# Optimization experiments

Hardware: AMD Instinct MI355X
Metric: run time of the kernel (lower is better)

## Reference

```python
import jax, jax.numpy as jnp
import numpy as np

N = 50000   # nodes
E = 800000  # edges
G = 64      # graphs in batch
H = 64      # hidden_dim
IN = 4      # input_dim (degree-derived features)


def setup_inputs() -> dict:
    key = jax.random.key(0)
    ks = jax.random.split(key, 9)
    src = jax.random.randint(ks[0], (E,), 0, N, dtype=jnp.int32)
    dst = jax.random.randint(ks[1], (E,), 0, N, dtype=jnp.int32)
    graph_ids = jnp.sort(jax.random.randint(ks[2], (N,), 0, G, dtype=jnp.int32))

    def glorot(k, shape):
        fan_in = shape[0]
        return jax.random.normal(k, shape, jnp.float32) / np.float32(np.sqrt(fan_in))

    return dict(
        src=src, dst=dst, graph_ids=graph_ids,
        W1=glorot(ks[3], (IN, H)), b1=jnp.zeros((H,), jnp.float32),
        W2=glorot(ks[4], (H, H)),  b2=jnp.zeros((H,), jnp.float32),
        W3=glorot(ks[5], (H, H)),  b3=jnp.zeros((H,), jnp.float32),
        W4=glorot(ks[6], (H, H)),  b4=jnp.zeros((H,), jnp.float32),
        Wout=glorot(ks[7], (H, 1)), bout=jnp.zeros((1,), jnp.float32),
    )


def _graph_conv(h, src, dst, norm_src, norm_dst, W, b):
    # DGL GraphConv, norm='both': D_dst^{-1/2} * A^T * (D_src^{-1/2} * h) @ W + b
    m = (h * norm_src)[src]                              # [E, F] gather
    agg = jax.ops.segment_sum(m, dst, num_segments=N)    # [N, F] scatter-add
    return (agg * norm_dst) @ W + b


def reference(src, dst, graph_ids, W1, b1, W2, b2, W3, b3, W4, b4, Wout, bout):
    ones_e = jnp.ones((E,), jnp.float32)
    in_deg = jax.ops.segment_sum(ones_e, dst, num_segments=N)   # [N]
    out_deg = jax.ops.segment_sum(ones_e, src, num_segments=N)  # [N]

    # degree-derived node features (exactly as in forward)
    h1 = in_deg[:, None]
    h2 = (in_deg - 3.0 > 0).astype(jnp.float32)[:, None]
    h3 = 3.0 / h1
    h4 = (in_deg - 4.0 > 0).astype(jnp.float32)[:, None]
    h_ = jnp.concatenate([h1, h2, h3, h4], axis=1)               # [N, 4]

    # symmetric norms (DGL clamps degree to >= 1)
    norm_src = jnp.clip(out_deg, 1.0, None)[:, None] ** -0.5     # [N, 1]
    norm_dst = jnp.clip(in_deg, 1.0, None)[:, None] ** -0.5      # [N, 1]

    h = jax.nn.relu(_graph_conv(h_, src, dst, norm_src, norm_dst, W1, b1))
    h = jax.nn.relu(_graph_conv(h, src, dst, norm_src, norm_dst, W2, b2))
    h = jax.nn.relu(_graph_conv(h, src, dst, norm_src, norm_dst, W3, b3))
    h = jax.nn.relu(_graph_conv(h, src, dst, norm_src, norm_dst, W4, b4))

    # dgl.mean_nodes: per-graph mean pooling
    node_counts = jax.ops.segment_sum(jnp.ones((N,), jnp.float32), graph_ids, num_segments=G)
    graph_emb = jax.ops.segment_sum(h, graph_ids, num_segments=G) / node_counts[:, None]

    # dropout = identity at inference
    return jax.nn.sigmoid(graph_emb @ Wout + bout)               # [G, 1]
```

## Files before the change

### kernel.cpp

```cpp
#include <hip/hip_runtime.h>
#include <hip/hip_fp8.h>
#include <math.h>

#define N_NODES 50000
#define N_EDGES 800000
#define NP 8
#define NS 64
#define PSZ (N_NODES / NP)
#define SSZ (N_EDGES / NS)
#define NB 196

typedef _Float16 half8 __attribute__((ext_vector_type(8)));
typedef float floatx4 __attribute__((ext_vector_type(4)));

__device__ __forceinline__ unsigned char f_to_fp8(float f) {
    __hip_fp8_e4m3 q(f);
    return (unsigned char)q.__x;
}
__device__ __forceinline__ float fp8_to_f(unsigned char u) {
    __hip_fp8_e4m3 q;
    q.__x = (__hip_fp8_storage_t)u;
    return (float)q;
}

__global__ __launch_bounds__(256) void hist_wt_kernel(const int* __restrict__ src,
                                                      const int* __restrict__ dst,
                                                      unsigned char* __restrict__ inpart,
                                                      unsigned char* __restrict__ outpart,
                                                      unsigned char* __restrict__ rank,
                                                      const float* __restrict__ W2,
                                                      const float* __restrict__ W3,
                                                      const float* __restrict__ W4,
                                                      _Float16* __restrict__ WT,
                                                      float* __restrict__ gacc) {
    __shared__ int h[PSZ + 2];
    if (blockIdx.x >= NP * NS) {
        int wb = blockIdx.x - NP * NS;
        if (wb < 48) {
            int i = wb * 256 + threadIdx.x;
            if (i < 3 * 4096) {
                int l = i >> 12;
                int r = i & 4095;
                int k = r >> 6, n = r & 63;
                const float* W = (l == 0) ? W2 : (l == 1) ? W3 : W4;
                WT[l * 4096 + n * 64 + k] = (_Float16)W[r];
            }
        } else {
            for (int i = threadIdx.x; i < 64 * 64 + 64; i += 256) gacc[i] = 0.0f;
        }
        return;
    }
    int p = blockIdx.x / NS, s = blockIdx.x % NS;
    for (int i = threadIdx.x; i < (PSZ + 2) / 4 + 1; i += 256)
        if (4 * i < PSZ + 2) ((int4*)h)[i] = make_int4(0, 0, 0, 0);
    __syncthreads();
    int lo = p * PSZ;
    int ebase = s * SSZ;
    const int4* d4 = (const int4*)(dst + ebase);
    const int4* s4 = (const int4*)(src + ebase);
    unsigned char* rk = rank + ebase;
    for (int i = threadIdx.x; i < SSZ / 4; i += 256) {
        int4 d = d4[i];
        int4 sv = s4[i];
        int t;
        t = d.x - lo;  if ((unsigned)t < PSZ) rk[4 * i + 0] = (unsigned char)(atomicAdd(&h[t], 1) & 0xffff);
        t = d.y - lo;  if ((unsigned)t < PSZ) rk[4 * i + 1] = (unsigned char)(atomicAdd(&h[t], 1) & 0xffff);
        t = d.z - lo;  if ((unsigned)t < PSZ) rk[4 * i + 2] = (unsigned char)(atomicAdd(&h[t], 1) & 0xffff);
        t = d.w - lo;  if ((unsigned)t < PSZ) rk[4 * i + 3] = (unsigned char)(atomicAdd(&h[t], 1) & 0xffff);
        t = sv.x - lo; if ((unsigned)t < PSZ) atomicAdd(&h[t], 0x10000);
        t = sv.y - lo; if ((unsigned)t < PSZ) atomicAdd(&h[t], 0x10000);
        t = sv.z - lo; if ((unsigned)t < PSZ) atomicAdd(&h[t], 0x10000);
        t = sv.w - lo; if ((unsigned)t < PSZ) atomicAdd(&h[t], 0x10000);
    }
    __syncthreads();
    unsigned char* ip = inpart + (size_t)s * N_NODES + lo;
    unsigned char* op = outpart + (size_t)s * N_NODES + lo;
    for (int i = threadIdx.x; i < PSZ / 2; i += 256) {
        int v0 = h[2 * i], v1 = h[2 * i + 1];
        uchar2 iv, ov;
        iv.x = (unsigned char)(v0 & 0xff);
        iv.y = (unsigned char)(v1 & 0xff);
        ov.x = (unsigned char)((v0 >> 16) & 0xff);
        ov.y = (unsigned char)((v1 >> 16) & 0xff);
        ((uchar2*)ip)[i] = iv;
        ((uchar2*)op)[i] = ov;
    }
}

__global__ void scan_block_feat_kernel(unsigned char* __restrict__ inpart,
                                       const unsigned char* __restrict__ outpart,
                                       const int* __restrict__ graph_ids,
                                       int* __restrict__ row_start, int* __restrict__ blk_sums,
                                       float* __restrict__ norm_src, float* __restrict__ norm_dst,
                                       uchar4* __restrict__ hs0, float* __restrict__ gcnt, int N) {
    __shared__ int ghist[64];
    if (threadIdx.x < 64) ghist[threadIdx.x] = 0;
    int i = blockIdx.x * 256 + threadIdx.x;
    int din_i = 0, dout_i = 0;
    if (i < N) {
        unsigned char run = 0;
#pragma unroll
        for (int s = 0; s < NS; ++s) {
            unsigned char c = inpart[(size_t)s * N_NODES + i];
            inpart[(size_t)s * N_NODES + i] = run;
            run = (unsigned char)(run + c);
            dout_i += outpart[(size_t)s * N_NODES + i];
        }
        din_i = (int)run;
        float din = (float)din_i;
        float dout = (float)dout_i;
        float ns = 1.0f / sqrtf(fmaxf(dout, 1.0f));
        float nd = 1.0f / sqrtf(fmaxf(din, 1.0f));
        norm_src[i] = ns;
        norm_dst[i] = nd;
        float h1 = din;
        float h2 = (din - 3.0f > 0.0f) ? 1.0f : 0.0f;
        float h3 = 3.0f / din;
        float h4 = (din - 4.0f > 0.0f) ? 1.0f : 0.0f;
        uchar4 q;
        q.x = f_to_fp8(h1 * ns);
        q.y = f_to_fp8(h2 * ns);
        q.z = f_to_fp8(h3 * ns);
        q.w = f_to_fp8(h4 * ns);
        hs0[i] = q;
    }
    __syncthreads();
    if (i < N) atomicAdd(&ghist[graph_ids[i]], 1);
    int lane = threadIdx.x & 63;
    int wid = threadIdx.x >> 6;
    int x = din_i;
#pragma unroll
    for (int off = 1; off < 64; off <<= 1) {
        int t = __shfl_up(x, off);
        if (lane >= off) x += t;
    }
    __shared__ int wsum[4];
    if (lane == 63) wsum[wid] = x;
    __syncthreads();
    int woff = 0;
    for (int w = 0; w < wid; ++w) woff += wsum[w];
    int incl = x + woff;
    if (i < N) row_start[i] = incl - din_i;
    if (threadIdx.x == 255) blk_sums[blockIdx.x] = incl;
    if (threadIdx.x < 64 && ghist[threadIdx.x] > 0)
        atomicAdd(&gcnt[threadIdx.x], (float)ghist[threadIdx.x]);
}

__global__ void row_add_kernel(int* __restrict__ row_start,
                               const int* __restrict__ blk_sums, int N) {
    __shared__ int sOff[256];
    int t = threadIdx.x;
    int v = (t < NB) ? blk_sums[t] : 0;
    int lane = t & 63;
    int wid = t >> 6;
    int x = v;
#pragma unroll
    for (int off = 1; off < 64; off <<= 1) {
        int tt = __shfl_up(x, off);
        if (lane >= off) x += tt;
    }
    __shared__ int wsum[4];
    if (lane == 63) wsum[wid] = x;
    __syncthreads();
    int woff = 0;
    for (int w = 0; w < wid; ++w) woff += wsum[w];
    sOff[t] = x + woff - v;
    __syncthreads();
    int i = blockIdx.x * 256 + threadIdx.x;
    if (blockIdx.x == 0 && threadIdx.x == 0) row_start[N] = N_EDGES;
    if (i < N) row_start[i] += sOff[blockIdx.x];
}

__global__ __launch_bounds__(256) void csr_fill_kernel(const int* __restrict__ src,
                                                       const int* __restrict__ dst,
                                                       const int* __restrict__ row_start,
                                                       const unsigned char* __restrict__ inpart,
                                                       const unsigned char* __restrict__ rank,
                                                       int* __restrict__ csr_src) {
    int i = blockIdx.x * 256 + threadIdx.x;
    if (i >= N_EDGES / 4) return;
    int4 d = ((const int4*)dst)[i];
    int4 sv = ((const int4*)src)[i];
    uchar4 rk = ((const uchar4*)rank)[i];
    int s = (4 * i) / SSZ;
    const unsigned char* pref = inpart + (size_t)s * N_NODES;
    csr_src[row_start[d.x] + (int)pref[d.x] + (int)rk.x] = sv.x;
    csr_src[row_start[d.y] + (int)pref[d.y] + (int)rk.y] = sv.y;
    csr_src[row_start[d.z] + (int)pref[d.z] + (int)rk.z] = sv.z;
    csr_src[row_start[d.w] + (int)pref[d.w] + (int)rk.w] = sv.w;
}

__global__ void conv4_kernel(const uchar4* __restrict__ hs0,
                             const int* __restrict__ row_start,
                             const int* __restrict__ csr_src,
                             const float* __restrict__ norm_src,
                             const float* __restrict__ norm_dst,
                             const float* __restrict__ W, const float* __restrict__ b,
                             unsigned char* __restrict__ out, int N) {
    __shared__ float sW[4 * 64];
    __shared__ float sb[64];
    sW[threadIdx.x] = W[threadIdx.x];
    if (threadIdx.x < 64) sb[threadIdx.x] = b[threadIdx.x];
    __syncthreads();
    int lane = threadIdx.x & 63;
    int wid = threadIdx.x >> 6;
    int v = blockIdx.x * 4 + wid;
    if (v >= N) return;
    int rs = row_start[v], re = row_start[v + 1];
    float ax = 0.f, ay = 0.f, az = 0.f, aw = 0.f;
    for (int e = rs + lane; e < re; e += 64) {
        uchar4 f = hs0[csr_src[e]];
        ax += fp8_to_f(f.x); ay += fp8_to_f(f.y);
        az += fp8_to_f(f.z); aw += fp8_to_f(f.w);
    }
#pragma unroll
    for (int off = 32; off; off >>= 1) {
        ax += __shfl_xor(ax, off);
        ay += __shfl_xor(ay, off);
        az += __shfl_xor(az, off);
        aw += __shfl_xor(aw, off);
    }
    float nd = norm_dst[v];
    float r = sb[lane] + nd * (ax * sW[lane] + ay * sW[64 + lane] +
                               az * sW[128 + lane] + aw * sW[192 + lane]);
    r = fmaxf(r, 0.0f) * norm_src[v];
    out[(size_t)v * 64 + lane] = f_to_fp8(r);
}

#define LOADIDX(MY, E0)  MY = csr_src[(E0) + (lane & 15)];

#define GATHER(T, MY)                                                   \
    _Pragma("unroll")                                                   \
    for (int j = 0; j < 16; ++j) {                                      \
        unsigned uu = (unsigned)__builtin_amdgcn_readlane(MY, j);       \
        if (uu >= (unsigned)N_NODES) uu = 0;                            \
        T[j] = hs_in[(uu << 6) + (unsigned)lane];                       \
    }

#define ACCUM(T)                                                        \
    _Pragma("unroll")                                                   \
    for (int j = 0; j < 16; ++j) {                                      \
        while (ecur == bound) {                                         \
            float ndc = __uint_as_float(                                \
                (unsigned)__builtin_amdgcn_readlane((int)nd8u, cur - vbase)); \
            sAgg[wavei][cur - vbase][lane] = (_Float16)(acc * ndc);     \
            acc = 0.0f;                                                 \
            ++cur;                                                      \
            bound = (cur < vend)                                        \
                        ? __builtin_amdgcn_readlane(rb8, cur - vbase)   \
                        : 0x7fffffff;                                   \
        }                                                               \
        acc += fp8_to_f(T[j]);                                          \
        ++ecur;                                                         \
    }

__global__ __launch_bounds__(256) void conv64_kernel(
        const unsigned char* __restrict__ hs_in,
        const int* __restrict__ row_start,
        const int* __restrict__ csr_src,
        const float* __restrict__ norm_src,
        const float* __restrict__ norm_dst,
        const _Float16* __restrict__ WT, const float* __restrict__ b,
        unsigned char* __restrict__ out8,
        const int* __restrict__ graph_ids, float* __restrict__ gacc,
        int do_pool, int N) {
    __shared__ _Float16 sAgg[4][16][72];
    const int lane = threadIdx.x & 63;
    const int wavei = __builtin_amdgcn_readfirstlane(threadIdx.x >> 6);
    const int vbase = blockIdx.x * 32 + wavei * 8;
    if (vbase >= N) return;

    const int vend = vbase + 8;
    const int rb8 = row_start[vbase + 1 + (lane & 7)];
    const unsigned nd8u = __float_as_uint(norm_dst[vbase + (lane & 7)]);
    const unsigned ns8u = __float_as_uint(norm_src[vbase + (lane & 7)]);
    const int rs = row_start[vbase];
    const int re = __builtin_amdgcn_readlane(rb8, 7);
    int cur = vbase;
    int bound = __builtin_amdgcn_readlane(rb8, 0);
    int ecur = rs;
    float acc = 0.0f;
    int nbp = (re - rs + 15) >> 4;
    int e = rs;
    int myA, myB;
    unsigned char tA[16], tB[16];

    if (nbp > 0) {
        LOADIDX(myA, e);
        GATHER(tA, myA);
        LOADIDX(myB, e + 16);
        int k = 0;
        while (k + 2 <= nbp) {
            GATHER(tB, myB);
            LOADIDX(myA, e + 32);
            ACCUM(tA);
            if (k + 2 < nbp) {
                GATHER(tA, myA);
                LOADIDX(myB, e + 48);
            }
            ACCUM(tB);
            k += 2; e += 32;
        }
        if (k < nbp) { ACCUM(tA); }
    }
    while (cur < vend) {
        float ndc = __uint_as_float(
            (unsigned)__builtin_amdgcn_readlane((int)nd8u, cur - vbase));
        sAgg[wavei][cur - vbase][lane] = (_Float16)(acc * ndc);
        acc = 0.0f;
        ++cur;
    }

    const int l15 = lane & 15;
    const int quad = lane >> 4;
    const _Float16* aRow = &sAgg[wavei][l15][quad * 8];
    half8 a0 = *(const half8*)(aRow);
    half8 a1 = *(const half8*)(aRow + 32);

    floatx4 c[4];
#pragma unroll
    for (int nt = 0; nt < 4; ++nt) c[nt] = (floatx4){0.f, 0.f, 0.f, 0.f};

#pragma unroll
    for (int nt = 0; nt < 4; ++nt) {
        const _Float16* bp = WT + ((size_t)(nt * 16 + l15)) * 64 + quad * 8;
        half8 b0 = *(const half8*)bp;
        half8 b1 = *(const half8*)(bp + 32);
        c[nt] = __builtin_amdgcn_mfma_f32_16x16x32_f16(a0, b0, c[nt], 0, 0, 0);
        c[nt] = __builtin_amdgcn_mfma_f32_16x16x32_f16(a1, b1, c[nt], 0, 0, 0);
    }

    if (do_pool) {
        int g0 = graph_ids[vbase];
        int g7 = graph_ids[vbase + 7];
        if (g0 == g7) {
#pragma unroll
            for (int nt = 0; nt < 4; ++nt) {
                float bias = b[nt * 16 + l15];
                float fsum = 0.0f;
                if (quad < 2) {
#pragma unroll
                    for (int r = 0; r < 4; ++r)
                        fsum += fmaxf(c[nt][r] + bias, 0.0f);
                }
                fsum += __shfl_xor(fsum, 16);
                if (quad == 0)
                    atomicAdd(&gacc[g0 * 64 + nt * 16 + l15], fsum);
            }
        } else {
#pragma unroll
            for (int nt = 0; nt < 4; ++nt) {
                float bias = b[nt * 16 + l15];
#pragma unroll
                for (int r = 0; r < 4; ++r) {
                    int m = quad * 4 + r;
                    if (m < 8) {
                        int v = vbase + m;
                        float val = fmaxf(c[nt][r] + bias, 0.0f);
                        atomicAdd(&gacc[graph_ids[v] * 64 + nt * 16 + l15], val);
                    }
                }
            }
        }
    } else {
#pragma unroll
        for (int nt = 0; nt < 4; ++nt) {
            float bias = b[nt * 16 + l15];
#pragma unroll
            for (int r = 0; r < 4; ++r) {
                int m = quad * 4 + r;
                int v = vbase + m;
                if (m < 8 && v < N) {
                    float nsv = __uint_as_float(
                        (unsigned)__builtin_amdgcn_readlane((int)ns8u, m));
                    float val = fmaxf(c[nt][r] + bias, 0.0f) * nsv;
                    out8[(size_t)v * 64 + nt * 16 + l15] = f_to_fp8(val);
                }
            }
        }
    }
}

__global__ void pool2_kernel(const float* __restrict__ gacc, const float* __restrict__ gcnt,
                             const float* __restrict__ Wout, const float* __restrict__ bout,
                             float* __restrict__ out) {
    int lane = threadIdx.x & 63;
    int g = blockIdx.x * 4 + (threadIdx.x >> 6);
    float p = (gacc[g * 64 + lane] / gcnt[g]) * Wout[lane];
#pragma unroll
    for (int off = 32; off; off >>= 1) p += __shfl_xor(p, off);
    if (lane == 0) out[g] = 1.0f / (1.0f + expf(-(p + bout[0])));
}

extern "C" void kernel_launch(void* const* d_in, const int* in_sizes, int n_in,
                              void* d_out, int out_size, void* d_ws, size_t ws_size,
                              hipStream_t stream) {
    const int* src = (const int*)d_in[0];
    const int* dst = (const int*)d_in[1];
    const int* graph_ids = (const int*)d_in[2];
    const float* W1 = (const float*)d_in[3];
    const float* b1 = (const float*)d_in[4];
    const float* W2 = (const float*)d_in[5];
    const float* b2 = (const float*)d_in[6];
    const float* W3 = (const float*)d_in[7];
    const float* b3 = (const float*)d_in[8];
    const float* W4 = (const float*)d_in[9];
    const float* b4 = (const float*)d_in[10];
    const float* Wout = (const float*)d_in[11];
    const float* bout = (const float*)d_in[12];
    float* out = (float*)d_out;

    const int N = N_NODES, E = N_EDGES;

    unsigned char* buf8A = (unsigned char*)d_ws;
    unsigned char* buf8B = buf8A + (size_t)N * 64;
    _Float16* WT   = (_Float16*)(buf8B + (size_t)N * 64);
    float* gacc = (float*)(WT + 3 * 4096);
    float* gcnt = gacc + 64 * 64;
    unsigned char* hs0 = (unsigned char*)(gcnt + 64);
    float* norm_src = (float*)(hs0 + (size_t)N * 4);
    float* norm_dst = norm_src + N;
    int* csr_src   = (int*)(norm_dst + N);
    int* row_start = csr_src + E;
    int* blk_sums  = row_start + (N + 1);
    unsigned char* inpart  = (unsigned char*)(blk_sums + NB + 1);
    unsigned char* outpart = inpart + (size_t)NS * N;
    unsigned char* rank    = outpart + (size_t)NS * N;

    hist_wt_kernel<<<NP * NS + 49, 256, 0, stream>>>(src, dst, inpart, outpart, rank,
                                                     W2, W3, W4, WT, gacc);
    scan_block_feat_kernel<<<NB, 256, 0, stream>>>(inpart, outpart, graph_ids,
                                                   row_start, blk_sums,
                                                   norm_src, norm_dst, (uchar4*)hs0, gcnt, N);
    row_add_kernel<<<NB, 256, 0, stream>>>(row_start, blk_sums, N);
    csr_fill_kernel<<<(E / 4 + 255) / 256, 256, 0, stream>>>(src, dst, row_start, inpart,
                                                             rank, csr_src);

    conv4_kernel<<<(N + 3) / 4, 256, 0, stream>>>((const uchar4*)hs0, row_start, csr_src,
                                                  norm_src, norm_dst, W1, b1, buf8A, N);
    const int CB = (N + 31) / 32;
    conv64_kernel<<<CB, 256, 0, stream>>>(buf8A, row_start, csr_src, norm_src, norm_dst,
                                          WT + 0 * 4096, b2, buf8B, graph_ids, gacc, 0, N);
    conv64_kernel<<<CB, 256, 0, stream>>>(buf8B, row_start, csr_src, norm_src, norm_dst,
                                          WT + 1 * 4096, b3, buf8A, graph_ids, gacc, 0, N);
    conv64_kernel<<<CB, 256, 0, stream>>>(buf8A, row_start, csr_src, norm_src, norm_dst,
                                          WT + 2 * 4096, b4, (unsigned char*)nullptr,
                                          graph_ids, gacc, 1, N);

    pool2_kernel<<<16, 256, 0, stream>>>(gacc, gcnt, Wout, bout, out);
}
```

Baseline: 212.5 us.

## Replace partitioned LDS histogram CSR build with global atomic counting and fill

Drops the partitioned shared-memory histogram with per-slice byte counts and ranks. Degrees are now counted with global atomics, and the CSR fill claims slots with atomicAdd on a write pointer array. A memset now zeroes the accumulators and degree arrays, and the scan reads degrees directly instead of walking 64 slices. This removes a large LDS-zeroing phase and the per-slice prefix work, but relies on contended global atomics and makes the neighbor order inside each row nondeterministic.

Measured after the change: 300.2 us. 1.41x slower.

```diff
diff --git a/kernel.cpp b/kernel.cpp
--- a/kernel.cpp
+++ b/kernel.cpp
@@ -4,11 +4,8 @@
 
 #define N_NODES 50000
 #define N_EDGES 800000
-#define NP 8
-#define NS 64
-#define PSZ (N_NODES / NP)
-#define SSZ (N_EDGES / NS)
 #define NB 196
+#define EQB 782
 
 typedef _Float16 half8 __attribute__((ext_vector_type(8)));
 typedef float floatx4 __attribute__((ext_vector_type(4)));
@@ -23,90 +20,52 @@
     return (float)q;
 }
 
-__global__ __launch_bounds__(256) void hist_wt_kernel(const int* __restrict__ src,
-                                                      const int* __restrict__ dst,
-                                                      unsigned char* __restrict__ inpart,
-                                                      unsigned char* __restrict__ outpart,
-                                                      unsigned char* __restrict__ rank,
-                                                      const float* __restrict__ W2,
-                                                      const float* __restrict__ W3,
-                                                      const float* __restrict__ W4,
-                                                      _Float16* __restrict__ WT,
-                                                      float* __restrict__ gacc) {
-    __shared__ int h[PSZ + 2];
-    if (blockIdx.x >= NP * NS) {
-        int wb = blockIdx.x - NP * NS;
-        if (wb < 48) {
-            int i = wb * 256 + threadIdx.x;
-            if (i < 3 * 4096) {
-                int l = i >> 12;
-                int r = i & 4095;
-                int k = r >> 6, n = r & 63;
-                const float* W = (l == 0) ? W2 : (l == 1) ? W3 : W4;
-                WT[l * 4096 + n * 64 + k] = (_Float16)W[r];
-            }
-        } else {
-            for (int i = threadIdx.x; i < 64 * 64 + 64; i += 256) gacc[i] = 0.0f;
+__global__ __launch_bounds__(256) void count_wt_kernel(const int* __restrict__ src,
+                                                       const int* __restrict__ dst,
+                                                       int* __restrict__ deg_in,
+                                                       int* __restrict__ deg_out,
+                                                       const float* __restrict__ W2,
+                                                       const float* __restrict__ W3,
+                                                       const float* __restrict__ W4,
+                                                       _Float16* __restrict__ WT) {
+    if (blockIdx.x >= EQB) {
+        int i = (blockIdx.x - EQB) * 256 + threadIdx.x;
+        if (i < 3 * 4096) {
+            int l = i >> 12;
+            int r = i & 4095;
+            int k = r >> 6, n = r & 63;
+            const float* W = (l == 0) ? W2 : (l == 1) ? W3 : W4;
+            WT[l * 4096 + n * 64 + k] = (_Float16)W[r];
         }
         return;
     }
-    int p = blockIdx.x / NS, s = blockIdx.x % NS;
-    for (int i = threadIdx.x; i < (PSZ + 2) / 4 + 1; i += 256)
-        if (4 * i < PSZ + 2) ((int4*)h)[i] = make_int4(0, 0, 0, 0);
-    __syncthreads();
-    int lo = p * PSZ;
-    int ebase = s * SSZ;
-    const int4* d4 = (const int4*)(dst + ebase);
-    const int4* s4 = (const int4*)(src + ebase);
-    unsigned char* rk = rank + ebase;
-    for (int i = threadIdx.x; i < SSZ / 4; i += 256) {
-        int4 d = d4[i];
-        int4 sv = s4[i];
-        int t;
-        t = d.x - lo;  if ((unsigned)t < PSZ) rk[4 * i + 0] = (unsigned char)(atomicAdd(&h[t], 1) & 0xffff);
-        t = d.y - lo;  if ((unsigned)t < PSZ) rk[4 * i + 1] = (unsigned char)(atomicAdd(&h[t], 1) & 0xffff);
-        t = d.z - lo;  if ((unsigned)t < PSZ) rk[4 * i + 2] = (unsigned char)(atomicAdd(&h[t], 1) & 0xffff);
-        t = d.w - lo;  if ((unsigned)t < PSZ) rk[4 * i + 3] = (unsigned char)(atomicAdd(&h[t], 1) & 0xffff);
-        t = sv.x - lo; if ((unsigned)t < PSZ) atomicAdd(&h[t], 0x10000);
-        t = sv.y - lo; if ((unsigned)t < PSZ) atomicAdd(&h[t], 0x10000);
-        t = sv.z - lo; if ((unsigned)t < PSZ) atomicAdd(&h[t], 0x10000);
-        t = sv.w - lo; if ((unsigned)t < PSZ) atomicAdd(&h[t], 0x10000);
-    }
-    __syncthreads();
-    unsigned char* ip = inpart + (size_t)s * N_NODES + lo;
-    unsigned char* op = outpart + (size_t)s * N_NODES + lo;
-    for (int i = threadIdx.x; i < PSZ / 2; i += 256) {
-        int v0 = h[2 * i], v1 = h[2 * i + 1];
-        uchar2 iv, ov;
-        iv.x = (unsigned char)(v0 & 0xff);
-        iv.y = (unsigned char)(v1 & 0xff);
-        ov.x = (unsigned char)((v0 >> 16) & 0xff);
-        ov.y = (unsigned char)((v1 >> 16) & 0xff);
-        ((uchar2*)ip)[i] = iv;
-        ((uchar2*)op)[i] = ov;
-    }
-}
-
-__global__ void scan_block_feat_kernel(unsigned char* __restrict__ inpart,
-                                       const unsigned char* __restrict__ outpart,
-                                       const int* __restrict__ graph_ids,
-                                       int* __restrict__ row_start, int* __restrict__ blk_sums,
-                                       float* __restrict__ norm_src, float* __restrict__ norm_dst,
-                                       uchar4* __restrict__ hs0, float* __restrict__ gcnt, int N) {
+    int i = blockIdx.x * 256 + threadIdx.x;
+    if (i >= N_EDGES / 4) return;
+    int4 d = ((const int4*)dst)[i];
+    int4 s = ((const int4*)src)[i];
+    atomicAdd(&deg_in[d.x], 1);
+    atomicAdd(&deg_in[d.y], 1);
+    atomicAdd(&deg_in[d.z], 1);
+    atomicAdd(&deg_in[d.w], 1);
+    atomicAdd(&deg_out[s.x], 1);
+    atomicAdd(&deg_out[s.y], 1);
+    atomicAdd(&deg_out[s.z], 1);
+    atomicAdd(&deg_out[s.w], 1);
+}
+
+__global__ void feat_scan_kernel(const int* __restrict__ deg_in,
+                                 const int* __restrict__ deg_out,
+                                 const int* __restrict__ graph_ids,
+                                 int* __restrict__ row_start, int* __restrict__ blk_sums,
+                                 float* __restrict__ norm_src, float* __restrict__ norm_dst,
+                                 uchar4* __restrict__ hs0, float* __restrict__ gcnt, int N) {
     __shared__ int ghist[64];
     if (threadIdx.x < 64) ghist[threadIdx.x] = 0;
     int i = blockIdx.x * 256 + threadIdx.x;
-    int din_i = 0, dout_i = 0;
+    int din_i = 0;
     if (i < N) {
-        unsigned char run = 0;
-#pragma unroll
-        for (int s = 0; s < NS; ++s) {
-            unsigned char c = inpart[(size_t)s * N_NODES + i];
-            inpart[(size_t)s * N_NODES + i] = run;
-            run = (unsigned char)(run + c);
-            dout_i += outpart[(size_t)s * N_NODES + i];
-        }
-        din_i = (int)run;
+        din_i = deg_in[i];
+        int dout_i = deg_out[i];
         float din = (float)din_i;
         float dout = (float)dout_i;
         float ns = 1.0f / sqrtf(fmaxf(dout, 1.0f));
@@ -147,7 +106,8 @@
 }
 
 __global__ void row_add_kernel(int* __restrict__ row_start,
-                               const int* __restrict__ blk_sums, int N) {
+                               const int* __restrict__ blk_sums,
+                               int* __restrict__ wptr, int N) {
     __shared__ int sOff[256];
     int t = threadIdx.x;
     int v = (t < NB) ? blk_sums[t] : 0;
@@ -168,26 +128,25 @@
     __syncthreads();
     int i = blockIdx.x * 256 + threadIdx.x;
     if (blockIdx.x == 0 && threadIdx.x == 0) row_start[N] = N_EDGES;
-    if (i < N) row_start[i] += sOff[blockIdx.x];
-}
-
-__global__ __launch_bounds__(256) void csr_fill_kernel(const int* __restrict__ src,
-                                                       const int* __restrict__ dst,
-                                                       const int* __restrict__ row_start,
-                                                       const unsigned char* __restrict__ inpart,
-                                                       const unsigned char* __restrict__ rank,
-                                                       int* __restrict__ csr_src) {
+    if (i < N) {
+        int rv = row_start[i] + sOff[blockIdx.x];
+        row_start[i] = rv;
+        wptr[i] = rv;
+    }
+}
+
+__global__ __launch_bounds__(256) void fill_kernel(const int* __restrict__ src,
+                                                   const int* __restrict__ dst,
+                                                   int* __restrict__ wptr,
+                                                   int* __restrict__ csr_src) {
     int i = blockIdx.x * 256 + threadIdx.x;
     if (i >= N_EDGES / 4) return;
     int4 d = ((const int4*)dst)[i];
     int4 sv = ((const int4*)src)[i];
-    uchar4 rk = ((const uchar4*)rank)[i];
-    int s = (4 * i) / SSZ;
-    const unsigned char* pref = inpart + (size_t)s * N_NODES;
-    csr_src[row_start[d.x] + (int)pref[d.x] + (int)rk.x] = sv.x;
-    csr_src[row_start[d.y] + (int)pref[d.y] + (int)rk.y] = sv.y;
-    csr_src[row_start[d.z] + (int)pref[d.z] + (int)rk.z] = sv.z;
-    csr_src[row_start[d.w] + (int)pref[d.w] + (int)rk.w] = sv.w;
+    csr_src[atomicAdd(&wptr[d.x], 1)] = sv.x;
+    csr_src[atomicAdd(&wptr[d.y], 1)] = sv.y;
+    csr_src[atomicAdd(&wptr[d.z], 1)] = sv.z;
+    csr_src[atomicAdd(&wptr[d.w], 1)] = sv.w;
 }
 
 __global__ void conv4_kernel(const uchar4* __restrict__ hs0,
@@ -415,26 +374,27 @@
     unsigned char* buf8A = (unsigned char*)d_ws;
     unsigned char* buf8B = buf8A + (size_t)N * 64;
     _Float16* WT   = (_Float16*)(buf8B + (size_t)N * 64);
-    float* gacc = (float*)(WT + 3 * 4096);
-    float* gcnt = gacc + 64 * 64;
-    unsigned char* hs0 = (unsigned char*)(gcnt + 64);
+    float* gacc    = (float*)(WT + 3 * 4096);
+    float* gcnt    = gacc + 64 * 64;
+    int*   deg_in  = (int*)(gcnt + 64);
+    int*   deg_out = deg_in + N;
+    size_t zbytes  = (size_t)(64 * 64 + 64 + 2 * N) * 4;
+    int*   wptr    = deg_out + N;
+    unsigned char* hs0 = (unsigned char*)(wptr + N);
     float* norm_src = (float*)(hs0 + (size_t)N * 4);
     float* norm_dst = norm_src + N;
     int* csr_src   = (int*)(norm_dst + N);
     int* row_start = csr_src + E;
     int* blk_sums  = row_start + (N + 1);
-    unsigned char* inpart  = (unsigned char*)(blk_sums + NB + 1);
-    unsigned char* outpart = inpart + (size_t)NS * N;
-    unsigned char* rank    = outpart + (size_t)NS * N;
-
-    hist_wt_kernel<<<NP * NS + 49, 256, 0, stream>>>(src, dst, inpart, outpart, rank,
-                                                     W2, W3, W4, WT, gacc);
-    scan_block_feat_kernel<<<NB, 256, 0, stream>>>(inpart, outpart, graph_ids,
-                                                   row_start, blk_sums,
-                                                   norm_src, norm_dst, (uchar4*)hs0, gcnt, N);
-    row_add_kernel<<<NB, 256, 0, stream>>>(row_start, blk_sums, N);
-    csr_fill_kernel<<<(E / 4 + 255) / 256, 256, 0, stream>>>(src, dst, row_start, inpart,
-                                                             rank, csr_src);
+
+    hipMemsetAsync(gacc, 0, zbytes, stream);
+    count_wt_kernel<<<EQB + 48, 256, 0, stream>>>(src, dst, deg_in, deg_out,
+                                                  W2, W3, W4, WT);
+    feat_scan_kernel<<<NB, 256, 0, stream>>>(deg_in, deg_out, graph_ids,
+                                             row_start, blk_sums,
+                                             norm_src, norm_dst, (uchar4*)hs0, gcnt, N);
+    row_add_kernel<<<NB, 256, 0, stream>>>(row_start, blk_sums, wptr, N);
+    fill_kernel<<<EQB, 256, 0, stream>>>(src, dst, wptr, csr_src);
 
     conv4_kernel<<<(N + 3) / 4, 256, 0, stream>>>((const uchar4*)hs0, row_start, csr_src,
                                                   norm_src, norm_dst, W1, b1, buf8A, N);
```

## Fuse final pooling into last conv via ticket counter and halve histogram partitions

Applied to the files above, without the earlier changes.

Removes the separate pool2 kernel launch: the last four waves to finish the final conv layer, found through an atomic ticket counter, compute the per-graph mean, output dot product and sigmoid. It also halves the number of node partitions in the histogram kernel, so each block covers twice the nodes with a larger shared-memory histogram. The ticket scheme relies on memory fences and atomic ordering for correctness. The larger LDS footprint and fewer blocks may lower occupancy in the histogram pass.

Result: slower. 309.9 us (+45.9%).

```diff
diff --git a/kernel.cpp b/kernel.cpp
--- a/kernel.cpp
+++ b/kernel.cpp
@@ -4,11 +4,12 @@
 
 #define N_NODES 50000
 #define N_EDGES 800000
-#define NP 8
+#define NP 4
 #define NS 64
 #define PSZ (N_NODES / NP)
 #define SSZ (N_EDGES / NS)
 #define NB 196
+#define NWAVES (N_NODES / 8)
 
 typedef _Float16 half8 __attribute__((ext_vector_type(8)));
 typedef float floatx4 __attribute__((ext_vector_type(4)));
@@ -33,7 +34,7 @@
                                                       const float* __restrict__ W4,
                                                       _Float16* __restrict__ WT,
                                                       float* __restrict__ gacc) {
-    __shared__ int h[PSZ + 2];
+    __shared__ int h[PSZ + 4];
     if (blockIdx.x >= NP * NS) {
         int wb = blockIdx.x - NP * NS;
         if (wb < 48) {
@@ -46,13 +47,13 @@
                 WT[l * 4096 + n * 64 + k] = (_Float16)W[r];
             }
         } else {
-            for (int i = threadIdx.x; i < 64 * 64 + 64; i += 256) gacc[i] = 0.0f;
+            for (int i = threadIdx.x; i < 64 * 64 + 64 + 4; i += 256) gacc[i] = 0.0f;
         }
         return;
     }
     int p = blockIdx.x / NS, s = blockIdx.x % NS;
-    for (int i = threadIdx.x; i < (PSZ + 2) / 4 + 1; i += 256)
-        if (4 * i < PSZ + 2) ((int4*)h)[i] = make_int4(0, 0, 0, 0);
+    for (int i = threadIdx.x; i < (PSZ + 4) / 4; i += 256)
+        ((int4*)h)[i] = make_int4(0, 0, 0, 0);
     __syncthreads();
     int lo = p * PSZ;
     int ebase = s * SSZ;
@@ -250,7 +251,7 @@
                         ? __builtin_amdgcn_readlane(rb8, cur - vbase)   \
                         : 0x7fffffff;                                   \
         }                                                               \
-        acc += fp8_to_f(T[j]);                                          \
+        acc += fp8_to_f(T[j]);                                         \
         ++ecur;                                                         \
     }
 
@@ -263,7 +264,10 @@
         const _Float16* __restrict__ WT, const float* __restrict__ b,
         unsigned char* __restrict__ out8,
         const int* __restrict__ graph_ids, float* __restrict__ gacc,
-        int do_pool, int N) {
+        int do_pool, int N,
+        const float* __restrict__ gcnt, const float* __restrict__ Wout,
+        const float* __restrict__ bout, float* __restrict__ gout,
+        int* __restrict__ ticket) {
     __shared__ _Float16 sAgg[4][16][72];
     const int lane = threadIdx.x & 63;
     const int wavei = __builtin_amdgcn_readfirstlane(threadIdx.x >> 6);
@@ -362,6 +366,22 @@
                 }
             }
         }
+        __threadfence();
+        int old = 0;
+        if (lane == 0) old = atomicAdd(ticket, 1);
+        old = __builtin_amdgcn_readfirstlane(old);
+        if (old >= NWAVES - 4) {
+            __threadfence();
+            int gbase = (old - (NWAVES - 4)) * 16;
+            for (int g = gbase; g < gbase + 16; ++g) {
+                float pv = __hip_atomic_load(&gacc[g * 64 + lane], __ATOMIC_RELAXED,
+                                             __HIP_MEMORY_SCOPE_AGENT);
+                float p = (pv / gcnt[g]) * Wout[lane];
+#pragma unroll
+                for (int off = 32; off; off >>= 1) p += __shfl_xor(p, off);
+                if (lane == 0) gout[g] = 1.0f / (1.0f + expf(-(p + bout[0])));
+            }
+        }
     } else {
 #pragma unroll
         for (int nt = 0; nt < 4; ++nt) {
@@ -379,17 +399,6 @@
             }
         }
     }
-}
-
-__global__ void pool2_kernel(const float* __restrict__ gacc, const float* __restrict__ gcnt,
-                             const float* __restrict__ Wout, const float* __restrict__ bout,
-                             float* __restrict__ out) {
-    int lane = threadIdx.x & 63;
-    int g = blockIdx.x * 4 + (threadIdx.x >> 6);
-    float p = (gacc[g * 64 + lane] / gcnt[g]) * Wout[lane];
-#pragma unroll
-    for (int off = 32; off; off >>= 1) p += __shfl_xor(p, off);
-    if (lane == 0) out[g] = 1.0f / (1.0f + expf(-(p + bout[0])));
 }
 
 extern "C" void kernel_launch(void* const* d_in, const int* in_sizes, int n_in,
@@ -417,7 +426,8 @@
     _Float16* WT   = (_Float16*)(buf8B + (size_t)N * 64);
     float* gacc = (float*)(WT + 3 * 4096);
     float* gcnt = gacc + 64 * 64;
-    unsigned char* hs0 = (unsigned char*)(gcnt + 64);
+    int*   ticket = (int*)(gcnt + 64);
+    unsigned char* hs0 = (unsigned char*)(ticket + 4);
     float* norm_src = (float*)(hs0 + (size_t)N * 4);
     float* norm_dst = norm_src + N;
     int* csr_src   = (int*)(norm_dst + N);
@@ -440,12 +450,13 @@
                                                   norm_src, norm_dst, W1, b1, buf8A, N);
     const int CB = (N + 31) / 32;
     conv64_kernel<<<CB, 256, 0, stream>>>(buf8A, row_start, csr_src, norm_src, norm_dst,
-                                          WT + 0 * 4096, b2, buf8B, graph_ids, gacc, 0, N);
+                                          WT + 0 * 4096, b2, buf8B, graph_ids, gacc, 0, N,
+                                          gcnt, Wout, bout, out, ticket);
     conv64_kernel<<<CB, 256, 0, stream>>>(buf8B, row_start, csr_src, norm_src, norm_dst,
-                                          WT + 1 * 4096, b3, buf8A, graph_ids, gacc, 0, N);
+                                          WT + 1 * 4096, b3, buf8A, graph_ids, gacc, 0, N,
+                                          gcnt, Wout, bout, out, ticket);
     conv64_kernel<<<CB, 256, 0, stream>>>(buf8A, row_start, csr_src, norm_src, norm_dst,
                                           WT + 2 * 4096, b4, (unsigned char*)nullptr,
-                                          graph_ids, gacc, 1, N);
-
-    pool2_kernel<<<16, 256, 0, stream>>>(gacc, gcnt, Wout, bout, out);
-}
+                                          graph_ids, gacc, 1, N,
+                                          gcnt, Wout, bout, out, ticket);
+}
```
